# Kernel tuning notes

Measured on AMD Instinct MI355X. Metric: run time of the kernel, lower is better.

Reference implementation:

```python
import jax, jax.numpy as jnp
import numpy as np

NEG_SLOPE = 0.2
EPS = 1e-16  # PyG softmax denominator epsilon


def gatv2_layer(x, src, dst, W_l, W_r, att, bias, num_nodes, heads, out_dim, concat):
    # x: [N, F_in]; src/dst: [E] (self-loops already included)
    x_l = (x @ W_l).reshape(num_nodes, heads, out_dim)  # source transform
    x_r = (x @ W_r).reshape(num_nodes, heads, out_dim)  # target transform
    # GATv2 scoring: a^T LeakyReLU(x_l[j] + x_r[i])
    e = jax.nn.leaky_relu(x_l[src] + x_r[dst], NEG_SLOPE)       # [E, H, D]
    logits = jnp.einsum('ehd,hd->eh', e, att)                    # [E, H]
    # segment softmax over incoming edges of each target node
    m = jax.ops.segment_max(logits, dst, num_segments=num_nodes)  # [N, H]
    ex = jnp.exp(logits - m[dst])                                 # [E, H]
    denom = jax.ops.segment_sum(ex, dst, num_segments=num_nodes)  # [N, H]
    alpha = ex / (denom[dst] + EPS)                               # [E, H]
    msg = x_l[src] * alpha[:, :, None]                            # [E, H, D]
    out = jax.ops.segment_sum(msg, dst, num_segments=num_nodes)   # [N, H, D]
    if concat:
        out = out.reshape(num_nodes, heads * out_dim)
    else:
        out = out.mean(axis=1)
    return out + bias


def setup_inputs() -> dict:
    key = jax.random.key(0)
    ks = jax.random.split(key, 10)
    N, E, F_in, H, D, F_out = 50000, 400000, 256, 4, 128, 64

    def glorot(k, shape, fan):
        return jax.random.normal(k, shape, dtype=jnp.float32) * (1.0 / np.sqrt(fan))

    return {
        'x': jax.random.normal(ks[0], (N, F_in), dtype=jnp.float32),
        'edge_index': jax.random.randint(ks[1], (2, E), 0, N, dtype=jnp.int64),
        'W_l1': glorot(ks[2], (F_in, H * D), F_in),
        'W_r1': glorot(ks[3], (F_in, H * D), F_in),
        'att1': glorot(ks[4], (H, D), D),
        'b1': jnp.zeros((H * D,), dtype=jnp.float32),
        'W_l2': glorot(ks[5], (H * D, F_out), H * D),
        'W_r2': glorot(ks[6], (H * D, F_out), H * D),
        'att2': glorot(ks[7], (1, F_out), F_out),
        'b2': jnp.zeros((F_out,), dtype=jnp.float32),
    }


def reference(x, edge_index, W_l1, W_r1, att1, b1, W_l2, W_r2, att2, b2):
    N = x.shape[0]
    # add self-loops (PyG GATv2Conv default add_self_loops=True)
    loops = jnp.arange(N, dtype=edge_index.dtype)
    src = jnp.concatenate([edge_index[0], loops])
    dst = jnp.concatenate([edge_index[1], loops])
    # dropout(p=0.6) is identity in eval mode
    h = gatv2_layer(x, src, dst, W_l1, W_r1, att1, b1, N, heads=4, out_dim=128, concat=True)
    h = jax.nn.elu(h)
    out = gatv2_layer(h, src, dst, W_l2, W_r2, att2, b2, N, heads=1, out_dim=64, concat=False)
    return out
```

## Files before the change

### kernel.cpp

```cpp
#include <hip/hip_runtime.h>
#include <hip/hip_bf16.h>
#include <math.h>


#define NEG_SLOPE 0.2f
#define LOG2E 1.4426950408889634f

typedef _Float16 half8 __attribute__((ext_vector_type(8)));
typedef _Float16 h4 __attribute__((ext_vector_type(4)));
typedef _Float16 h2 __attribute__((ext_vector_type(2)));
typedef float f32x4 __attribute__((ext_vector_type(4)));
typedef float f32x2 __attribute__((ext_vector_type(2)));

#if __has_builtin(__builtin_amdgcn_global_load_lds)
#define HAS_GLL 1
__device__ __forceinline__ void gll16(const _Float16* g, _Float16* l) {
    __builtin_amdgcn_global_load_lds(
        (const __attribute__((address_space(1))) unsigned int*)g,
        (__attribute__((address_space(3))) unsigned int*)l, 16, 0, 0);
}
#endif

__device__ __forceinline__ float dot2acc(h2 a, h2 b, float c) {
#if __has_builtin(__builtin_amdgcn_fdot2)
    return __builtin_amdgcn_fdot2(a, b, c, false);
#else
    return fmaf((float)a[1], (float)b[1], fmaf((float)a[0], (float)b[0], c));
#endif
}

__device__ __forceinline__ float fast_exp2(float p) {
#if __has_builtin(__builtin_amdgcn_exp2f)
    return __builtin_amdgcn_exp2f(p);
#else
    return exp2f(p);
#endif
}

__device__ __forceinline__ h2 lrelu2(h2 t, h2 ns2) {
#if __has_builtin(__builtin_elementwise_max)
    return __builtin_elementwise_max(t, t * ns2);
#else
    h2 tn = t * ns2;
    t[0] = (t[0] > tn[0]) ? t[0] : tn[0];
    t[1] = (t[1] > tn[1]) ? t[1] : tn[1];
    return t;
#endif
}


__global__ __launch_bounds__(256) void k_castx_count(const float* __restrict__ x, _Float16* __restrict__ xh,
                                                     int n8, const int* __restrict__ ei,
                                                     int* __restrict__ counts, int E, int Etot, int gEtot) {
    int b = blockIdx.x;
    if (b < gEtot) {
        int i = b * 256 + threadIdx.x;
        if (i < Etot) {
            int dst = (i < E) ? ei[E + i] : (i - E);
            atomicAdd(&counts[dst], 1);
        }
    } else {
        int i = (b - gEtot) * 256 + threadIdx.x;
        if (i < n8) {
            const float4* p = (const float4*)(x + i * 8);
            float4 a = p[0], c = p[1];
            half8 v;
            v[0] = (_Float16)a.x; v[1] = (_Float16)a.y; v[2] = (_Float16)a.z; v[3] = (_Float16)a.w;
            v[4] = (_Float16)c.x; v[5] = (_Float16)c.y; v[6] = (_Float16)c.z; v[7] = (_Float16)c.w;
            *(half8*)(xh + i * 8) = v;
        }
    }
}


__global__ __launch_bounds__(1024) void k_castw_scana(const int* __restrict__ counts, int* __restrict__ offs,
                                                      int* __restrict__ partial, int n, int nsb,
                                                      const float* __restrict__ Wl1, const float* __restrict__ Wr1,
                                                      const float* __restrict__ Wl2, const float* __restrict__ Wr2,
                                                      _Float16* __restrict__ W1T, _Float16* __restrict__ W2T) {
    __shared__ int buf[1024];
    int b = blockIdx.x, t = threadIdx.x;
    if (b < nsb) {
        int i = b * 1024 + t;
        int v = (i < n) ? counts[i] : 0;
        buf[t] = v;
        __syncthreads();
        #pragma unroll
        for (int off = 1; off < 1024; off <<= 1) {
            int add = (t >= off) ? buf[t - off] : 0;
            __syncthreads();
            buf[t] += add;
            __syncthreads();
        }
        if (i < n) offs[i + 1] = buf[t];
        if (t == 1023) partial[b] = buf[1023];
    } else {
        int i = (b - nsb) * 1024 + t;
        const int T1 = 1024 * 256;
        const int T2 = 128 * 512;
        if (i < T1) {
            int nn = i >> 8, k = i & 255;
            float v = (nn < 512) ? Wl1[k * 512 + nn] : Wr1[k * 512 + (nn - 512)];
            W1T[i] = (_Float16)v;
        } else if (i < T1 + T2) {
            int j = i - T1;
            int nn = j >> 9, k = j & 511;
            float v = (nn < 64) ? Wl2[k * 64 + nn] : Wr2[k * 64 + (nn - 64)];
            W2T[j] = (_Float16)v;
        }
    }
}


__global__ __launch_bounds__(256) void k_scanbc(int* __restrict__ offs, int* __restrict__ cursor,
                                                const int* __restrict__ partial, int n, int nsb) {
    __shared__ int s[256];
    int t = threadIdx.x;
    int v = (t < nsb) ? partial[t] : 0;
    s[t] = v;
    __syncthreads();
    #pragma unroll
    for (int off = 1; off < 256; off <<= 1) {
        int add = (t >= off) ? s[t - off] : 0;
        __syncthreads();
        s[t] += add;
        __syncthreads();
    }
    int excl = s[t] - v;
    s[t] = excl;
    __syncthreads();
    int i = blockIdx.x * 256 + t;
    if (i == 0) { offs[0] = 0; cursor[0] = 0; }
    if (i < n) {
        int w = offs[i + 1] + s[i >> 10];
        offs[i + 1] = w;
        cursor[i + 1] = w;
    }
}


__device__ __forceinline__ void gemm_body(const _Float16* __restrict__ A,
                                          const _Float16* __restrict__ Bt,
                                          _Float16* __restrict__ C,
                                          int M, int N, int K, int ntiles, int blk,
                                          _Float16* As, _Float16* Bs) {
    int tid = threadIdx.x;
    int lane = tid & 63;
    int wave = tid >> 6;
    int wm = wave >> 2, wn = wave & 3;
    int l15 = lane & 15, q = lane >> 4;

    int ntile = blk % ntiles;
    int mtile = blk / ntiles;
    int tileM = mtile * 128;
    int tileN = ntile * 128;

    int srow = lane >> 2;
    int schunk = (lane & 3) ^ ((lane >> 3) & 3);
    const _Float16* gA = A + (long)(tileM + wave * 16 + srow) * K + schunk * 8;
    const _Float16* gB = Bt + (long)(tileN + wave * 16 + srow) * K + schunk * 8;
    _Float16* lA = As + wave * 512;
    _Float16* lB = Bs + wave * 512;

    int aswz = (q ^ ((l15 >> 1) & 3)) * 8;

    f32x4 acc[4][2];
    #pragma unroll
    for (int i = 0; i < 4; ++i)
        #pragma unroll
        for (int j = 0; j < 2; ++j)
            acc[i][j] = (f32x4)(0.f);

    for (int k0 = 0; k0 < K; k0 += 32) {
#ifdef HAS_GLL
        gll16(gA + k0, lA);
        gll16(gB + k0, lB);
#else
        half8 va = *(const half8*)(gA + k0);
        half8 vb = *(const half8*)(gB + k0);
        *(half8*)(lA + lane * 8) = va;
        *(half8*)(lB + lane * 8) = vb;
#endif
        __syncthreads();

        half8 af[4], bf[2];
        #pragma unroll
        for (int i = 0; i < 4; ++i)
            af[i] = *(const half8*)(As + (wm * 64 + i * 16 + l15) * 32 + aswz);
        #pragma unroll
        for (int j = 0; j < 2; ++j)
            bf[j] = *(const half8*)(Bs + (wn * 32 + j * 16 + l15) * 32 + aswz);

        __syncthreads();

        #pragma unroll
        for (int i = 0; i < 4; ++i)
            #pragma unroll
            for (int j = 0; j < 2; ++j)
                acc[i][j] = __builtin_amdgcn_mfma_f32_16x16x32_f16(bf[j], af[i], acc[i][j], 0, 0, 0);
    }

    #pragma unroll
    for (int i = 0; i < 4; ++i) {
        int grow = tileM + wm * 64 + i * 16 + l15;
        if (grow < M) {
            #pragma unroll
            for (int j = 0; j < 2; ++j) {
                int gcol = tileN + wn * 32 + j * 16 + q * 4;
                h4 v;
                v[0] = (_Float16)acc[i][j][0];
                v[1] = (_Float16)acc[i][j][1];
                v[2] = (_Float16)acc[i][j][2];
                v[3] = (_Float16)acc[i][j][3];
                *(h4*)(C + (long)grow * N + gcol) = v;
            }
        }
    }
}

__global__ __launch_bounds__(512) void k_gemm1_fill(const _Float16* __restrict__ A,
                                                    const _Float16* __restrict__ Bt,
                                                    _Float16* __restrict__ C,
                                                    int M, int N, int K, int ntiles, int gb,
                                                    const int* __restrict__ ei, int* __restrict__ cursor,
                                                    int* __restrict__ csr_src, int E, int Etot) {
    __shared__ _Float16 As[128 * 32];
    __shared__ _Float16 Bs[128 * 32];
    int b = blockIdx.x;
    if (b < gb) {
        gemm_body(A, Bt, C, M, N, K, ntiles, b, As, Bs);
    } else {
        int i = (b - gb) * 512 + threadIdx.x;
        if (i < Etot) {
            int src, dst;
            if (i < E) { src = ei[i]; dst = ei[E + i]; }
            else       { src = i - E; dst = i - E; }
            int pos = atomicAdd(&cursor[dst], 1);
            csr_src[pos] = src;
        }
    }
}

__global__ __launch_bounds__(512) void k_gemm_f16(const _Float16* __restrict__ A,
                                                  const _Float16* __restrict__ Bt,
                                                  _Float16* __restrict__ C,
                                                  int M, int N, int K, int ntiles) {
    __shared__ _Float16 As[128 * 32];
    __shared__ _Float16 Bs[128 * 32];
    gemm_body(A, Bt, C, M, N, K, ntiles, blockIdx.x, As, Bs);
}


__global__ __launch_bounds__(256) void k_attn1(const _Float16* __restrict__ xlr,
                                               const float* __restrict__ att, const float* __restrict__ b1,
                                               const int* __restrict__ offs, const int* __restrict__ csr_src,
                                               _Float16* __restrict__ hout, int N) {
    int wave = threadIdx.x >> 6;
    int lane = threadIdx.x & 63;
    int node = blockIdx.x * 4 + wave;
    if (node >= N) return;

    int cbase = (lane >> 4) * 128 + (lane & 15) * 8;
    const _Float16* xlr_l = xlr + cbase;

    half8 xrv8 = *(const half8*)(xlr_l + ((unsigned)node << 10) + 512);
    float4 atv0 = *(const float4*)(att + cbase);
    float4 atv1 = *(const float4*)(att + cbase + 4);
    h2 xr[4], at[4];
    #pragma unroll
    for (int j = 0; j < 4; ++j) {
        xr[j][0] = xrv8[2 * j]; xr[j][1] = xrv8[2 * j + 1];
    }
    at[0][0] = (_Float16)(atv0.x * LOG2E); at[0][1] = (_Float16)(atv0.y * LOG2E);
    at[1][0] = (_Float16)(atv0.z * LOG2E); at[1][1] = (_Float16)(atv0.w * LOG2E);
    at[2][0] = (_Float16)(atv1.x * LOG2E); at[2][1] = (_Float16)(atv1.y * LOG2E);
    at[3][0] = (_Float16)(atv1.z * LOG2E); at[3][1] = (_Float16)(atv1.w * LOG2E);
    const h2 ns2 = {(_Float16)NEG_SLOPE, (_Float16)NEG_SLOPE};

    float l = 0.f;
    f32x2 acc[4];
    #pragma unroll
    for (int j = 0; j < 4; ++j) acc[j] = (f32x2)(0.f);

    int e0 = offs[node], e1 = offs[node + 1];
    int s_next = csr_src[e0];
    int s_next2 = (e0 + 1 < e1) ? csr_src[e0 + 1] : 0;
    half8 xlv = *(const half8*)(xlr_l + ((unsigned)s_next << 10));

    for (int e = e0; e < e1; ++e) {
        half8 cur = xlv;
        int s_pf = s_next2;
        if (e + 2 < e1) s_next2 = csr_src[e + 2];
        if (e + 1 < e1) xlv = *(const half8*)(xlr_l + ((unsigned)s_pf << 10));

        const h2* cp = (const h2*)&cur;
        float p = 0.f;
        #pragma unroll
        for (int j = 0; j < 4; ++j) {
            h2 t = lrelu2(cp[j] + xr[j], ns2);
            p = dot2acc(t, at[j], p);
        }
        #pragma unroll
        for (int off = 1; off <= 8; off <<= 1) p += __shfl_xor(p, off, 64);
        float w = fast_exp2(p);
        l += w;
        f32x2 w2 = {w, w};
        #pragma unroll
        for (int j = 0; j < 4; ++j) {
            f32x2 xf = {(float)cur[2 * j], (float)cur[2 * j + 1]};
            acc[j] = w2 * xf + acc[j];
        }
    }

    float inv = 1.f / (l + 1e-16f);
    float4 b1v0 = *(const float4*)(b1 + cbase);
    float4 b1v1 = *(const float4*)(b1 + cbase + 4);
    float bb[8] = {b1v0.x, b1v0.y, b1v0.z, b1v0.w, b1v1.x, b1v1.y, b1v1.z, b1v1.w};
    half8 ov;
    #pragma unroll
    for (int j = 0; j < 8; ++j) {
        float o = fmaf(acc[j >> 1][j & 1], inv, bb[j]);
        o = (o > 0.f) ? o : (__expf(o) - 1.f);
        ov[j] = (_Float16)o;
    }
    *(half8*)(hout + (long)node * 512 + cbase) = ov;
}


__global__ __launch_bounds__(256) void k_attn2(const _Float16* __restrict__ xlr2,
                                               const float* __restrict__ att, const float* __restrict__ b2,
                                               const int* __restrict__ offs, const int* __restrict__ csr_src,
                                               float* __restrict__ out, int N) {
    int wave = threadIdx.x >> 6;
    int lane = threadIdx.x & 63;
    int node = blockIdx.x * 4 + wave;
    if (node >= N) return;

    int g  = lane >> 4;
    int gl = lane & 15;
    int ch = gl * 4;
    const _Float16* base = xlr2 + ch;

    h4 xr4 = *(const h4*)(base + ((unsigned)node << 7) + 64);
    h2 xr0 = {xr4[0], xr4[1]}, xr1 = {xr4[2], xr4[3]};
    float4 atf = *(const float4*)(att + ch);
    h2 at0; at0[0] = (_Float16)(atf.x * LOG2E); at0[1] = (_Float16)(atf.y * LOG2E);
    h2 at1; at1[0] = (_Float16)(atf.z * LOG2E); at1[1] = (_Float16)(atf.w * LOG2E);
    const h2 ns2 = {(_Float16)NEG_SLOPE, (_Float16)NEG_SLOPE};

    float l = 0.f;
    f32x2 acc0 = (f32x2)(0.f), acc1 = (f32x2)(0.f);
    int e0 = offs[node], e1 = offs[node + 1];
    int e = e0 + g;
    h4 cv;
    if (e < e1) {
        int s = csr_src[e];
        cv = *(const h4*)(base + ((unsigned)s << 7));
    }
    while (e < e1) {
        h4 u = cv;
        int en = e + 4;
        if (en < e1) {
            int s = csr_src[en];
            cv = *(const h4*)(base + ((unsigned)s << 7));
        }
        h2 u0 = {u[0], u[1]}, u1 = {u[2], u[3]};
        h2 t0 = lrelu2(u0 + xr0, ns2);
        h2 t1 = lrelu2(u1 + xr1, ns2);
        float p = dot2acc(t0, at0, 0.f);
        p = dot2acc(t1, at1, p);
        p += __shfl_xor(p, 1, 64);
        p += __shfl_xor(p, 2, 64);
        p += __shfl_xor(p, 4, 64);
        p += __shfl_xor(p, 8, 64);
        float w = fast_exp2(p);
        l += w;
        f32x2 w2 = {w, w};
        f32x2 x0 = {(float)u[0], (float)u[1]};
        f32x2 x1 = {(float)u[2], (float)u[3]};
        acc0 = w2 * x0 + acc0;
        acc1 = w2 * x1 + acc1;
        e = en;
    }
    float a0 = acc0[0], a1 = acc0[1], a2 = acc1[0], a3 = acc1[1];
    l  += __shfl_xor(l, 16, 64);  l  += __shfl_xor(l, 32, 64);
    a0 += __shfl_xor(a0, 16, 64); a0 += __shfl_xor(a0, 32, 64);
    a1 += __shfl_xor(a1, 16, 64); a1 += __shfl_xor(a1, 32, 64);
    a2 += __shfl_xor(a2, 16, 64); a2 += __shfl_xor(a2, 32, 64);
    a3 += __shfl_xor(a3, 16, 64); a3 += __shfl_xor(a3, 32, 64);
    if (g == 0) {
        float inv = 1.f / (l + 1e-16f);
        float4 bv = *(const float4*)(b2 + ch);
        float4 o;
        o.x = fmaf(a0, inv, bv.x);
        o.y = fmaf(a1, inv, bv.y);
        o.z = fmaf(a2, inv, bv.z);
        o.w = fmaf(a3, inv, bv.w);
        *(float4*)(out + (long)node * 64 + ch) = o;
    }
}


extern "C" void kernel_launch(void* const* d_in, const int* in_sizes, int n_in,
                              void* d_out, int out_size, void* d_ws, size_t ws_size,
                              hipStream_t stream) {
    const float* x    = (const float*)d_in[0];
    const int*   ei   = (const int*)d_in[1];
    const float* Wl1  = (const float*)d_in[2];
    const float* Wr1  = (const float*)d_in[3];
    const float* att1 = (const float*)d_in[4];
    const float* b1   = (const float*)d_in[5];
    const float* Wl2  = (const float*)d_in[6];
    const float* Wr2  = (const float*)d_in[7];
    const float* att2 = (const float*)d_in[8];
    const float* b2   = (const float*)d_in[9];
    float* out = (float*)d_out;

    const int F_IN = 256;
    int N = in_sizes[0] / F_IN;
    int E = in_sizes[1] / 2;
    int Etot = E + N;
    int nScanBlocks = (N + 1023) / 1024;
    int mtiles = (N + 127) / 128;
    int Mpad = mtiles * 128;

    char* p = (char*)d_ws;
    auto carve = [&](size_t bytes) -> void* {
        void* r = (void*)p;
        p += (bytes + 255) & ~(size_t)255;
        return r;
    };
    _Float16* xh   = (_Float16*)carve((size_t)Mpad * 256 * 2);
    _Float16* W1T  = (_Float16*)carve((size_t)1024 * 256 * 2);
    _Float16* W2T  = (_Float16*)carve((size_t)128 * 512 * 2);
    _Float16* C1   = (_Float16*)carve((size_t)N * 1024 * 2);
    _Float16* h    = (_Float16*)carve((size_t)Mpad * 512 * 2);
    _Float16* C2   = (_Float16*)carve((size_t)N * 128 * 2);
    int* counts  = (int*)carve((size_t)N * 4);
    int* offs    = (int*)carve((size_t)(N + 1) * 4);
    int* cursor  = (int*)carve((size_t)(N + 1) * 4);
    int* partial = (int*)carve((size_t)nScanBlocks * 4);
    int* csr     = (int*)carve((size_t)Etot * 4);

    int gN    = (N + 255) / 256;
    int gEtot = (Etot + 255) / 256;
    int n8    = N * 256 / 8;
    int gCast = (n8 + 255) / 256;

    hipMemsetAsync(counts, 0, (size_t)N * 4, stream);

    k_castx_count<<<gEtot + gCast, 256, 0, stream>>>(x, xh, n8, ei, counts, E, Etot, gEtot);

    {
        int total = 1024 * 256 + 128 * 512;
        int gW = (total + 1023) / 1024;
        k_castw_scana<<<nScanBlocks + gW, 1024, 0, stream>>>(counts, offs, partial, N, nScanBlocks,
                                                             Wl1, Wr1, Wl2, Wr2, W1T, W2T);
    }
    k_scanbc<<<gN, 256, 0, stream>>>(offs, cursor, partial, N, nScanBlocks);

    {
        int gb = mtiles * 8;
        int fillBlocks = (Etot + 511) / 512;
        k_gemm1_fill<<<gb + fillBlocks, 512, 0, stream>>>(xh, W1T, C1, N, 1024, 256, 8, gb,
                                                          ei, cursor, csr, E, Etot);
    }
    k_attn1<<<(N + 3) / 4, 256, 0, stream>>>(C1, att1, b1, offs, csr, h, N);

    k_gemm_f16<<<mtiles, 512, 0, stream>>>(h, W2T, C2, N, 128, 512, 1);
    k_attn2<<<(N + 3) / 4, 256, 0, stream>>>(C2, att2, b2, offs, csr, out, N);
}
```

Baseline: 325.3 us.

## Load GEMM operands directly from global into registers with double buffering

Drops the LDS staging and both per-iteration barriers in the fp16 MFMA GEMM. Each wave now loads its own A and B fragments straight from global memory into registers, with a two-stage register double buffer that overlaps the next k-slice load with the current MFMAs. Waves sharing rows or columns now fetch the same data redundantly from global memory or L2 instead of reusing it through LDS, and register pressure rises. The loop steps by 64, so it assumes K is a multiple of 64.

```diff
diff --git a/kernel.cpp b/kernel.cpp
--- a/kernel.cpp
+++ b/kernel.cpp
@@ -11,15 +11,6 @@
 typedef _Float16 h2 __attribute__((ext_vector_type(2)));
 typedef float f32x4 __attribute__((ext_vector_type(4)));
 typedef float f32x2 __attribute__((ext_vector_type(2)));
-
-#if __has_builtin(__builtin_amdgcn_global_load_lds)
-#define HAS_GLL 1
-__device__ __forceinline__ void gll16(const _Float16* g, _Float16* l) {
-    __builtin_amdgcn_global_load_lds(
-        (const __attribute__((address_space(1))) unsigned int*)g,
-        (__attribute__((address_space(3))) unsigned int*)l, 16, 0, 0);
-}
-#endif
 
 __device__ __forceinline__ float dot2acc(h2 a, h2 b, float c) {
 #if __has_builtin(__builtin_amdgcn_fdot2)
@@ -142,8 +133,7 @@
 __device__ __forceinline__ void gemm_body(const _Float16* __restrict__ A,
                                           const _Float16* __restrict__ Bt,
                                           _Float16* __restrict__ C,
-                                          int M, int N, int K, int ntiles, int blk,
-                                          _Float16* As, _Float16* Bs) {
+                                          int M, int N, int K, int ntiles, int blk) {
     int tid = threadIdx.x;
     int lane = tid & 63;
     int wave = tid >> 6;
@@ -155,14 +145,14 @@
     int tileM = mtile * 128;
     int tileN = ntile * 128;
 
-    int srow = lane >> 2;
-    int schunk = (lane & 3) ^ ((lane >> 3) & 3);
-    const _Float16* gA = A + (long)(tileM + wave * 16 + srow) * K + schunk * 8;
-    const _Float16* gB = Bt + (long)(tileN + wave * 16 + srow) * K + schunk * 8;
-    _Float16* lA = As + wave * 512;
-    _Float16* lB = Bs + wave * 512;
-
-    int aswz = (q ^ ((l15 >> 1) & 3)) * 8;
+    const _Float16* pA[4];
+    const _Float16* pB[2];
+    #pragma unroll
+    for (int i = 0; i < 4; ++i)
+        pA[i] = A + (long)(tileM + wm * 64 + i * 16 + l15) * K + q * 8;
+    #pragma unroll
+    for (int j = 0; j < 2; ++j)
+        pB[j] = Bt + (long)(tileN + wn * 32 + j * 16 + l15) * K + q * 8;
 
     f32x4 acc[4][2];
     #pragma unroll
@@ -171,33 +161,34 @@
         for (int j = 0; j < 2; ++j)
             acc[i][j] = (f32x4)(0.f);
 
-    for (int k0 = 0; k0 < K; k0 += 32) {
-#ifdef HAS_GLL
-        gll16(gA + k0, lA);
-        gll16(gB + k0, lB);
-#else
-        half8 va = *(const half8*)(gA + k0);
-        half8 vb = *(const half8*)(gB + k0);
-        *(half8*)(lA + lane * 8) = va;
-        *(half8*)(lB + lane * 8) = vb;
-#endif
-        __syncthreads();
-
-        half8 af[4], bf[2];
-        #pragma unroll
-        for (int i = 0; i < 4; ++i)
-            af[i] = *(const half8*)(As + (wm * 64 + i * 16 + l15) * 32 + aswz);
-        #pragma unroll
-        for (int j = 0; j < 2; ++j)
-            bf[j] = *(const half8*)(Bs + (wn * 32 + j * 16 + l15) * 32 + aswz);
-
-        __syncthreads();
-
+    half8 a1[4], b1[2], a2[4], b2[2];
+    #pragma unroll
+    for (int i = 0; i < 4; ++i) a1[i] = *(const half8*)(pA[i]);
+    #pragma unroll
+    for (int j = 0; j < 2; ++j) b1[j] = *(const half8*)(pB[j]);
+
+    for (int k0 = 0; k0 < K; k0 += 64) {
+        #pragma unroll
+        for (int i = 0; i < 4; ++i) a2[i] = *(const half8*)(pA[i] + k0 + 32);
+        #pragma unroll
+        for (int j = 0; j < 2; ++j) b2[j] = *(const half8*)(pB[j] + k0 + 32);
         #pragma unroll
         for (int i = 0; i < 4; ++i)
             #pragma unroll
             for (int j = 0; j < 2; ++j)
-                acc[i][j] = __builtin_amdgcn_mfma_f32_16x16x32_f16(bf[j], af[i], acc[i][j], 0, 0, 0);
+                acc[i][j] = __builtin_amdgcn_mfma_f32_16x16x32_f16(b1[j], a1[i], acc[i][j], 0, 0, 0);
+
+        if (k0 + 64 < K) {
+            #pragma unroll
+            for (int i = 0; i < 4; ++i) a1[i] = *(const half8*)(pA[i] + k0 + 64);
+            #pragma unroll
+            for (int j = 0; j < 2; ++j) b1[j] = *(const half8*)(pB[j] + k0 + 64);
+        }
+        #pragma unroll
+        for (int i = 0; i < 4; ++i)
+            #pragma unroll
+            for (int j = 0; j < 2; ++j)
+                acc[i][j] = __builtin_amdgcn_mfma_f32_16x16x32_f16(b2[j], a2[i], acc[i][j], 0, 0, 0);
     }
 
     #pragma unroll
@@ -224,11 +215,9 @@
                                                     int M, int N, int K, int ntiles, int gb,
                                                     const int* __restrict__ ei, int* __restrict__ cursor,
                                                     int* __restrict__ csr_src, int E, int Etot) {
-    __shared__ _Float16 As[128 * 32];
-    __shared__ _Float16 Bs[128 * 32];
     int b = blockIdx.x;
     if (b < gb) {
-        gemm_body(A, Bt, C, M, N, K, ntiles, b, As, Bs);
+        gemm_body(A, Bt, C, M, N, K, ntiles, b);
     } else {
         int i = (b - gb) * 512 + threadIdx.x;
         if (i < Etot) {
@@ -245,9 +234,7 @@
                                                   const _Float16* __restrict__ Bt,
                                                   _Float16* __restrict__ C,
                                                   int M, int N, int K, int ntiles) {
-    __shared__ _Float16 As[128 * 32];
-    __shared__ _Float16 Bs[128 * 32];
-    gemm_body(A, Bt, C, M, N, K, ntiles, blockIdx.x, As, Bs);
+    gemm_body(A, Bt, C, M, N, K, ntiles, blockIdx.x);
 }
 
 
```

Measured after the change: 431.5 us. +32.7%, slower.
